# Optimization experiments

Hardware: AMD Instinct MI355X
Metric: run time of the kernel (lower is better)

## Reference

```python
import jax, jax.numpy as jnp
import numpy as np

B, S, DIN, D = 16, 1024, 64, 64

def setup_inputs() -> dict:
    key = jax.random.key(0)
    kx, kq, kk, kv, kaK, kaV = jax.random.split(key, 6)
    w_scale = 1.0 / np.sqrt(DIN)
    x = jax.random.normal(kx, (B, S, DIN), dtype=jnp.float32)
    Wq = jax.random.normal(kq, (DIN, D), dtype=jnp.float32) * w_scale
    Wk = jax.random.normal(kk, (DIN, D), dtype=jnp.float32) * w_scale
    Wv = jax.random.normal(kv, (DIN, D), dtype=jnp.float32) * w_scale
    # relative-position bias tables alpha_K/alpha_V: [S, S, D]
    alpha_K = jax.random.normal(kaK, (S, S, D), dtype=jnp.float32) * 0.02
    alpha_V = jax.random.normal(kaV, (S, S, D), dtype=jnp.float32) * 0.02
    return {"x": x, "Wq": Wq, "Wk": Wk, "Wv": Wv,
            "alpha_K": alpha_K, "alpha_V": alpha_V}

def reference(x, Wq, Wk, Wv, alpha_K, alpha_V):
    # Relation-aware self-attention (Shaw et al. style), vectorized form of
    # the original per-query loop:
    #   score[b,i,j] = q[b,i] . (k[b,j] + alpha_K[i,j]) / sqrt(D)
    #   z[b,i]       = sum_j softmax_j(score)[b,i,j] * (v[b,j] + alpha_V[i,j])
    d = Wq.shape[1]
    inv_sqrt_d = 1.0 / np.sqrt(d)
    q = jnp.einsum('bsf,fd->bsd', x, Wq)
    k = jnp.einsum('bsf,fd->bsd', x, Wk)
    v = jnp.einsum('bsf,fd->bsd', x, Wv)
    scores = (jnp.einsum('bid,bjd->bij', q, k)
              + jnp.einsum('bid,ijd->bij', q, alpha_K)) * inv_sqrt_d
    attn = jax.nn.softmax(scores, axis=-1)  # [B, S, S]
    z = (jnp.einsum('bij,bjd->bid', attn, v)
         + jnp.einsum('bij,ijd->bid', attn, alpha_V))
    return z, attn
```

## Files before the change

kernel.cpp:

```cpp
#include <hip/hip_runtime.h>
#include <hip/hip_fp16.h>
#include <hip/hip_bf16.h>


typedef unsigned short u16;
typedef __attribute__((ext_vector_type(8))) short bhalf8;
typedef __attribute__((ext_vector_type(4))) float fx4;

__device__ __forceinline__ short b16(float f) {
  __hip_bfloat16 h = __float2bfloat16(f);
  return *reinterpret_cast<short*>(&h);
}

__device__ __forceinline__ bhalf8 pack8(float4 a, float4 b) {
  bhalf8 r;
  r[0] = b16(a.x); r[1] = b16(a.y); r[2] = b16(a.z); r[3] = b16(a.w);
  r[4] = b16(b.x); r[5] = b16(b.y); r[6] = b16(b.z); r[7] = b16(b.w);
  return r;
}

__global__ __launch_bounds__(256) void k_proj(
    const float* __restrict__ x, const float* __restrict__ Wq,
    const float* __restrict__ Wk, const float* __restrict__ Wv,
    u16* __restrict__ qbf, u16* __restrict__ kbf, float* __restrict__ vf)
{
  __shared__ float wl[3 * 4096];
  const int t = threadIdx.x;
  for (int c = t; c < 4096; c += 256) {
    wl[c] = Wq[c]; wl[4096 + c] = Wk[c]; wl[8192 + c] = Wv[c];
  }
  __syncthreads();
  const int row = blockIdx.x * 64 + (t >> 2);
  const int dbase = (t & 3) * 16;
  float xr[64];
  const float4* xp = (const float4*)(x + (size_t)row * 64);
#pragma unroll
  for (int c = 0; c < 16; ++c) {
    float4 v = xp[c];
    xr[4*c] = v.x; xr[4*c+1] = v.y; xr[4*c+2] = v.z; xr[4*c+3] = v.w;
  }
  float aq[16], ak[16], av[16];
#pragma unroll
  for (int m = 0; m < 16; ++m) { aq[m] = 0.f; ak[m] = 0.f; av[m] = 0.f; }
#pragma unroll
  for (int f = 0; f < 64; ++f) {
    const float xv = xr[f];
    const float* wq = wl + f * 64 + dbase;
#pragma unroll
    for (int m = 0; m < 16; ++m) {
      aq[m] = fmaf(xv, wq[m], aq[m]);
      ak[m] = fmaf(xv, wq[4096 + m], ak[m]);
      av[m] = fmaf(xv, wq[8192 + m], av[m]);
    }
  }
  union { u16 u[16]; uint4 q[2]; } pq, pk;
#pragma unroll
  for (int m = 0; m < 16; ++m) { pq.u[m] = (u16)b16(aq[m]); pk.u[m] = (u16)b16(ak[m]); }
  const size_t o = (size_t)row * 64 + dbase;
  *(uint4*)(qbf + o) = pq.q[0]; *(uint4*)(qbf + o + 8) = pq.q[1];
  *(uint4*)(kbf + o) = pk.q[0]; *(uint4*)(kbf + o + 8) = pk.q[1];
  float4* vo = (float4*)(vf + o);
  vo[0] = make_float4(av[0], av[1], av[2], av[3]);
  vo[1] = make_float4(av[4], av[5], av[6], av[7]);
  vo[2] = make_float4(av[8], av[9], av[10], av[11]);
  vo[3] = make_float4(av[12], av[13], av[14], av[15]);
}

__global__ __launch_bounds__(256) void k_qk(
    const u16* __restrict__ qbf, const u16* __restrict__ kbf, __half* __restrict__ qkw)
{
  const int t = threadIdx.x, l = t & 63, w = t >> 6;
  const int b = blockIdx.x & 15, it = blockIdx.x >> 4;
  const int lr = l & 15, lg = l >> 4;
  const int i0 = it * 64 + w * 16;
  const u16* qp = qbf + (size_t)(b * 1024 + i0 + lr) * 64 + lg * 8;
  bhalf8 a0 = *(const bhalf8*)(qp);
  bhalf8 a1 = *(const bhalf8*)(qp + 32);
  for (int jt = 0; jt < 64; ++jt) {
    const int j0 = jt * 16;
    const u16* kp = kbf + (size_t)(b * 1024 + j0 + lr) * 64 + lg * 8;
    bhalf8 b0 = *(const bhalf8*)(kp);
    bhalf8 b1 = *(const bhalf8*)(kp + 32);
    fx4 acc = {0.f, 0.f, 0.f, 0.f};
    acc = __builtin_amdgcn_mfma_f32_16x16x32_bf16(a0, b0, acc, 0, 0, 0);
    acc = __builtin_amdgcn_mfma_f32_16x16x32_bf16(a1, b1, acc, 0, 0, 0);
#pragma unroll
    for (int r = 0; r < 4; ++r) {
      const int i = i0 + lg * 4 + r;
      qkw[((size_t)i * 16 + b) * 1024 + j0 + lr] = __float2half(acc[r]);
    }
  }
}

#define SLD2 516
#define PADJ 40
__global__ __launch_bounds__(256, 4) void k_core(
    const float* __restrict__ aK, const float* __restrict__ aV,
    const u16* __restrict__ qbf, const __half* __restrict__ qkw,
    float* __restrict__ attn_out, float* __restrict__ za)
{
  __shared__ __align__(16) float sl[16 * SLD2];
  __shared__ __align__(16) u16 vt[64 * PADJ];
  __shared__ float stats[64];
  const int i = blockIdx.x;
  const int t = threadIdx.x, l = t & 63, w = t >> 6;
  const int lr = l & 15, lg = l >> 4;

  const u16* qp = qbf + (size_t)(lr * 1024 + i) * 64 + lg * 8;
  bhalf8 a0 = *(const bhalf8*)(qp);
  bhalf8 a1 = *(const bhalf8*)(qp + 32);

  fx4 zacc = {0.f, 0.f, 0.f, 0.f};

  const int jA = t >> 4;
  const int dA = (t & 15) * 4;

  for (int h = 0; h < 2; ++h) {
    const __half* qk = qkw + (size_t)i * 16384 + h * 512;
    for (int c = t; c < 1024; c += 256) {
      const int b = c >> 6;
      const int j8 = (c & 63) * 8;
      uint4 u = *(const uint4*)(qk + (size_t)b * 1024 + j8);
      const __half2* hh = (const __half2*)&u;
      float2 f0 = __half22float2(hh[0]);
      float2 f1 = __half22float2(hh[1]);
      float2 f2 = __half22float2(hh[2]);
      float2 f3 = __half22float2(hh[3]);
      float* dst = sl + b * SLD2 + j8;
      *(float4*)(dst)     = make_float4(f0.x, f0.y, f1.x, f1.y);
      *(float4*)(dst + 4) = make_float4(f2.x, f2.y, f3.x, f3.y);
    }
    __syncthreads();

    for (int tt = 0; tt < 8; ++tt) {
      const int j0 = (w + tt * 4) * 16;
      const float* ap = aK + ((size_t)i * 1024 + h * 512 + j0 + lr) * 64 + lg * 8;
      float4 c0 = *(const float4*)(ap);
      float4 c1 = *(const float4*)(ap + 4);
      float4 c2 = *(const float4*)(ap + 32);
      float4 c3 = *(const float4*)(ap + 36);
      fx4 acc = {0.f, 0.f, 0.f, 0.f};
      acc = __builtin_amdgcn_mfma_f32_16x16x32_bf16(a0, pack8(c0, c1), acc, 0, 0, 0);
      acc = __builtin_amdgcn_mfma_f32_16x16x32_bf16(a1, pack8(c2, c3), acc, 0, 0, 0);
#pragma unroll
      for (int r = 0; r < 4; ++r)
        sl[(lg * 4 + r) * SLD2 + j0 + lr] += acc[r];
    }
    __syncthreads();

    if (h == 0) {
#pragma unroll
      for (int rr = 0; rr < 4; ++rr) {
        const int row = w * 4 + rr;
        float* rp = sl + row * SLD2;
        float4 x0 = *(const float4*)(rp + l * 8);
        float4 x1 = *(const float4*)(rp + l * 8 + 4);
        float v8[8] = {x0.x, x0.y, x0.z, x0.w, x1.x, x1.y, x1.z, x1.w};
        float mx = -3.0e30f;
#pragma unroll
        for (int c = 0; c < 8; ++c) mx = fmaxf(mx, v8[c]);
#pragma unroll
        for (int off = 32; off; off >>= 1) mx = fmaxf(mx, __shfl_xor(mx, off));
        float e8[8]; float sum = 0.f;
#pragma unroll
        for (int c = 0; c < 8; ++c) { e8[c] = __expf((v8[c] - mx) * 0.125f); sum += e8[c]; }
        float* ao = attn_out + ((size_t)row * 1024 + i) * 1024;
        *(float4*)(ao + l * 8)     = make_float4(e8[0], e8[1], e8[2], e8[3]);
        *(float4*)(ao + l * 8 + 4) = make_float4(e8[4], e8[5], e8[6], e8[7]);
        bhalf8 eb;
#pragma unroll
        for (int c = 0; c < 8; ++c) eb[c] = b16(e8[c]);
        *(bhalf8*)((u16*)rp + l * 8) = eb;
#pragma unroll
        for (int off = 32; off; off >>= 1) sum += __shfl_xor(sum, off);
        if (l == 0) { stats[row] = mx; stats[16 + row] = sum; }
      }
    } else {
#pragma unroll
      for (int rr = 0; rr < 4; ++rr) {
        const int row = w * 4 + rr;
        float* rp = sl + row * SLD2;
        float4 x0 = *(const float4*)(rp + l * 8);
        float4 x1 = *(const float4*)(rp + l * 8 + 4);
        float v8[8] = {x0.x, x0.y, x0.z, x0.w, x1.x, x1.y, x1.z, x1.w};
        float mx = -3.0e30f;
#pragma unroll
        for (int c = 0; c < 8; ++c) mx = fmaxf(mx, v8[c]);
#pragma unroll
        for (int off = 32; off; off >>= 1) mx = fmaxf(mx, __shfl_xor(mx, off));
        const float m1 = stats[row];
        const float m  = fmaxf(m1, mx);
        const float corr = __expf((m1 - m) * 0.125f);
        float e8[8]; float sum = 0.f;
#pragma unroll
        for (int c = 0; c < 8; ++c) { e8[c] = __expf((v8[c] - m) * 0.125f); sum += e8[c]; }
        bhalf8 eb;
#pragma unroll
        for (int c = 0; c < 8; ++c) eb[c] = b16(e8[c]);
        *(bhalf8*)((u16*)rp + l * 8) = eb;
#pragma unroll
        for (int off = 32; off; off >>= 1) sum += __shfl_xor(sum, off);
        const float inv = 1.0f / (stats[16 + row] * corr + sum);
        float* ao = attn_out + ((size_t)row * 1024 + i) * 1024 + 512;
        *(float4*)(ao + l * 8)     = make_float4(e8[0]*inv, e8[1]*inv, e8[2]*inv, e8[3]*inv);
        *(float4*)(ao + l * 8 + 4) = make_float4(e8[4]*inv, e8[5]*inv, e8[6]*inv, e8[7]*inv);
        if (l == 0) { stats[32 + row] = corr; stats[48 + row] = inv; }
      }
    }
    __syncthreads();

    if (h == 1) {
#pragma unroll
      for (int r = 0; r < 4; ++r) zacc[r] *= stats[32 + lg * 4 + r];
    }
    float4 pa, pb;
    {
      const float* ap = aV + ((size_t)i * 1024 + h * 512 + jA) * 64 + dA;
      pa = *(const float4*)(ap);
      pb = *(const float4*)(ap + 1024);
    }
    for (int it = 0; it < 16; ++it) {
      __syncthreads();
      vt[(dA + 0) * PADJ + jA] = (u16)b16(pa.x);
      vt[(dA + 1) * PADJ + jA] = (u16)b16(pa.y);
      vt[(dA + 2) * PADJ + jA] = (u16)b16(pa.z);
      vt[(dA + 3) * PADJ + jA] = (u16)b16(pa.w);
      vt[(dA + 0) * PADJ + jA + 16] = (u16)b16(pb.x);
      vt[(dA + 1) * PADJ + jA + 16] = (u16)b16(pb.y);
      vt[(dA + 2) * PADJ + jA + 16] = (u16)b16(pb.z);
      vt[(dA + 3) * PADJ + jA + 16] = (u16)b16(pb.w);
      if (it < 15) {
        const float* ap = aV + ((size_t)i * 1024 + h * 512 + (it + 1) * 32 + jA) * 64 + dA;
        pa = *(const float4*)(ap);
        pb = *(const float4*)(ap + 1024);
      }
      __syncthreads();
      bhalf8 ea = *(const bhalf8*)((const u16*)(sl + (size_t)lr * SLD2) + it * 32 + lg * 8);
      bhalf8 bv = *(const bhalf8*)(vt + (w * 16 + lr) * PADJ + lg * 8);
      zacc = __builtin_amdgcn_mfma_f32_16x16x32_bf16(ea, bv, zacc, 0, 0, 0);
    }
    __syncthreads();
  }

#pragma unroll
  for (int r = 0; r < 4; ++r) {
    const int b = lg * 4 + r;
    za[((size_t)i * 16 + b) * 64 + w * 16 + lr] = zacc[r] * stats[48 + b];
  }

#pragma unroll
  for (int rr = 0; rr < 4; ++rr) {
    const int row = w * 4 + rr;
    const float f = stats[32 + row] * stats[48 + row];
    float* ao = attn_out + ((size_t)row * 1024 + i) * 1024;
    float4 u0 = *(const float4*)(ao + l * 8);
    float4 u1 = *(const float4*)(ao + l * 8 + 4);
    *(float4*)(ao + l * 8)     = make_float4(u0.x*f, u0.y*f, u0.z*f, u0.w*f);
    *(float4*)(ao + l * 8 + 4) = make_float4(u1.x*f, u1.y*f, u1.z*f, u1.w*f);
  }
}

__global__ __launch_bounds__(256) void k_zv(
    const float* __restrict__ attn, const float* __restrict__ vf,
    const float* __restrict__ za, float* __restrict__ zout)
{
  __shared__ __align__(16) u16 vt[64 * 40];
  const int t = threadIdx.x, l = t & 63, w = t >> 6;
  const int b = blockIdx.x & 15, it = blockIdx.x >> 4;
  const int lr = l & 15, lg = l >> 4;
  const int iw = it * 64 + w * 16;
  fx4 acc[4];
#pragma unroll
  for (int n = 0; n < 4; ++n) acc[n] = (fx4){0.f, 0.f, 0.f, 0.f};
  const int jl = t >> 3;
  const int c0 = (t & 7) * 8;
  for (int ks = 0; ks < 32; ++ks) {
    const int j0 = ks * 32;
    const float* vp = vf + (size_t)(b * 1024 + j0 + jl) * 64 + c0;
    float4 v0 = *(const float4*)(vp);
    float4 v1 = *(const float4*)(vp + 4);
    __syncthreads();
    vt[(c0 + 0) * 40 + jl] = (u16)b16(v0.x);
    vt[(c0 + 1) * 40 + jl] = (u16)b16(v0.y);
    vt[(c0 + 2) * 40 + jl] = (u16)b16(v0.z);
    vt[(c0 + 3) * 40 + jl] = (u16)b16(v0.w);
    vt[(c0 + 4) * 40 + jl] = (u16)b16(v1.x);
    vt[(c0 + 5) * 40 + jl] = (u16)b16(v1.y);
    vt[(c0 + 6) * 40 + jl] = (u16)b16(v1.z);
    vt[(c0 + 7) * 40 + jl] = (u16)b16(v1.w);
    __syncthreads();
    const float* apr = attn + (size_t)(b * 1024 + iw + lr) * 1024 + j0 + lg * 8;
    float4 t0 = *(const float4*)(apr);
    float4 t1 = *(const float4*)(apr + 4);
    bhalf8 af = pack8(t0, t1);
#pragma unroll
    for (int n = 0; n < 4; ++n) {
      bhalf8 bf = *(const bhalf8*)(vt + (n * 16 + lr) * 40 + lg * 8);
      acc[n] = __builtin_amdgcn_mfma_f32_16x16x32_bf16(af, bf, acc[n], 0, 0, 0);
    }
  }
#pragma unroll
  for (int n = 0; n < 4; ++n) {
#pragma unroll
    for (int r = 0; r < 4; ++r) {
      const int i = iw + lg * 4 + r;
      const int dd = n * 16 + lr;
      zout[((size_t)b * 1024 + i) * 64 + dd] = acc[n][r] + za[((size_t)i * 16 + b) * 64 + dd];
    }
  }
}

extern "C" void kernel_launch(void* const* d_in, const int* in_sizes, int n_in,
                              void* d_out, int out_size, void* d_ws, size_t ws_size,
                              hipStream_t stream)
{
  const float* x  = (const float*)d_in[0];
  const float* Wq = (const float*)d_in[1];
  const float* Wk = (const float*)d_in[2];
  const float* Wv = (const float*)d_in[3];
  const float* aK = (const float*)d_in[4];
  const float* aV = (const float*)d_in[5];
  float* zout = (float*)d_out;
  float* attn_out = zout + (size_t)16 * 1024 * 64;

  char* ws = (char*)d_ws;
  u16*    qbf = (u16*)(ws);
  u16*    kbf = (u16*)(ws + (size_t)2  * 1024 * 1024);
  float*  vf  = (float*)(ws + (size_t)4  * 1024 * 1024);
  float*  za  = (float*)(ws + (size_t)8  * 1024 * 1024);
  __half* qkw = (__half*)(ws + (size_t)12 * 1024 * 1024);

  hipLaunchKernelGGL(k_proj, dim3(256),  dim3(256), 0, stream, x, Wq, Wk, Wv, qbf, kbf, vf);
  hipLaunchKernelGGL(k_qk,   dim3(256),  dim3(256), 0, stream, qbf, kbf, qkw);
  hipLaunchKernelGGL(k_core, dim3(1024), dim3(256), 0, stream, aK, aV, qbf, qkw, attn_out, za);
  hipLaunchKernelGGL(k_zv,   dim3(256),  dim3(256), 0, stream, attn_out, vf, za, zout);
}
```

Before: 225.8 us.

## Fuse QK bias load into softmax and make aV staging per-warp without barriers

The separate pass that loaded the q·k scores into shared memory, along with its barrier, is removed. The MFMA result now overwrites the tile, and the fp16 q·k values are added in registers during the softmax pass. The aV transpose staging is repartitioned so each warp writes only the 16 d-columns it later reads, which removes the two __syncthreads per iteration of the 16-step loop. This relies on intra-wavefront ordering of LDS writes and reads, and the per-warp loads are narrower (64-byte strips per row), which may reduce memory coalescing.

```diff
diff --git a/kernel.cpp b/kernel.cpp
--- a/kernel.cpp
+++ b/kernel.cpp
@@ -112,26 +112,7 @@
 
   fx4 zacc = {0.f, 0.f, 0.f, 0.f};
 
-  const int jA = t >> 4;
-  const int dA = (t & 15) * 4;
-
   for (int h = 0; h < 2; ++h) {
-    const __half* qk = qkw + (size_t)i * 16384 + h * 512;
-    for (int c = t; c < 1024; c += 256) {
-      const int b = c >> 6;
-      const int j8 = (c & 63) * 8;
-      uint4 u = *(const uint4*)(qk + (size_t)b * 1024 + j8);
-      const __half2* hh = (const __half2*)&u;
-      float2 f0 = __half22float2(hh[0]);
-      float2 f1 = __half22float2(hh[1]);
-      float2 f2 = __half22float2(hh[2]);
-      float2 f3 = __half22float2(hh[3]);
-      float* dst = sl + b * SLD2 + j8;
-      *(float4*)(dst)     = make_float4(f0.x, f0.y, f1.x, f1.y);
-      *(float4*)(dst + 4) = make_float4(f2.x, f2.y, f3.x, f3.y);
-    }
-    __syncthreads();
-
     for (int tt = 0; tt < 8; ++tt) {
       const int j0 = (w + tt * 4) * 16;
       const float* ap = aK + ((size_t)i * 1024 + h * 512 + j0 + lr) * 64 + lg * 8;
@@ -144,7 +125,7 @@
       acc = __builtin_amdgcn_mfma_f32_16x16x32_bf16(a1, pack8(c2, c3), acc, 0, 0, 0);
 #pragma unroll
       for (int r = 0; r < 4; ++r)
-        sl[(lg * 4 + r) * SLD2 + j0 + lr] += acc[r];
+        sl[(lg * 4 + r) * SLD2 + j0 + lr] = acc[r];
     }
     __syncthreads();
 
@@ -153,9 +134,16 @@
       for (int rr = 0; rr < 4; ++rr) {
         const int row = w * 4 + rr;
         float* rp = sl + row * SLD2;
+        uint4 qv = *(const uint4*)(qkw + ((size_t)i * 16 + row) * 1024 + l * 8);
+        const __half2* hh = (const __half2*)&qv;
+        float2 f0 = __half22float2(hh[0]);
+        float2 f1 = __half22float2(hh[1]);
+        float2 f2 = __half22float2(hh[2]);
+        float2 f3 = __half22float2(hh[3]);
         float4 x0 = *(const float4*)(rp + l * 8);
         float4 x1 = *(const float4*)(rp + l * 8 + 4);
-        float v8[8] = {x0.x, x0.y, x0.z, x0.w, x1.x, x1.y, x1.z, x1.w};
+        float v8[8] = {x0.x + f0.x, x0.y + f0.y, x0.z + f1.x, x0.w + f1.y,
+                       x1.x + f2.x, x1.y + f2.y, x1.z + f3.x, x1.w + f3.y};
         float mx = -3.0e30f;
 #pragma unroll
         for (int c = 0; c < 8; ++c) mx = fmaxf(mx, v8[c]);
@@ -180,9 +168,16 @@
       for (int rr = 0; rr < 4; ++rr) {
         const int row = w * 4 + rr;
         float* rp = sl + row * SLD2;
+        uint4 qv = *(const uint4*)(qkw + ((size_t)i * 16 + row) * 1024 + 512 + l * 8);
+        const __half2* hh = (const __half2*)&qv;
+        float2 f0 = __half22float2(hh[0]);
+        float2 f1 = __half22float2(hh[1]);
+        float2 f2 = __half22float2(hh[2]);
+        float2 f3 = __half22float2(hh[3]);
         float4 x0 = *(const float4*)(rp + l * 8);
         float4 x1 = *(const float4*)(rp + l * 8 + 4);
-        float v8[8] = {x0.x, x0.y, x0.z, x0.w, x1.x, x1.y, x1.z, x1.w};
+        float v8[8] = {x0.x + f0.x, x0.y + f0.y, x0.z + f1.x, x0.w + f1.y,
+                       x1.x + f2.x, x1.y + f2.y, x1.z + f3.x, x1.w + f3.y};
         float mx = -3.0e30f;
 #pragma unroll
         for (int c = 0; c < 8; ++c) mx = fmaxf(mx, v8[c]);
@@ -213,30 +208,29 @@
 #pragma unroll
       for (int r = 0; r < 4; ++r) zacc[r] *= stats[32 + lg * 4 + r];
     }
-    float4 pa, pb;
-    {
-      const float* ap = aV + ((size_t)i * 1024 + h * 512 + jA) * 64 + dA;
-      pa = *(const float4*)(ap);
-      pb = *(const float4*)(ap + 1024);
-    }
+    const int jj = l >> 2;
+    const int cc = (l & 3) * 4;
+    const float* avbase = aV + ((size_t)i * 1024 + h * 512) * 64 + w * 16 + cc;
+    float4 pa = *(const float4*)(avbase + (size_t)jj * 64);
+    float4 pb = *(const float4*)(avbase + (size_t)(jj + 16) * 64);
     for (int it = 0; it < 16; ++it) {
-      __syncthreads();
-      vt[(dA + 0) * PADJ + jA] = (u16)b16(pa.x);
-      vt[(dA + 1) * PADJ + jA] = (u16)b16(pa.y);
-      vt[(dA + 2) * PADJ + jA] = (u16)b16(pa.z);
-      vt[(dA + 3) * PADJ + jA] = (u16)b16(pa.w);
-      vt[(dA + 0) * PADJ + jA + 16] = (u16)b16(pb.x);
-      vt[(dA + 1) * PADJ + jA + 16] = (u16)b16(pb.y);
-      vt[(dA + 2) * PADJ + jA + 16] = (u16)b16(pb.z);
-      vt[(dA + 3) * PADJ + jA + 16] = (u16)b16(pb.w);
+      float4 ca = pa, cb = pb;
       if (it < 15) {
-        const float* ap = aV + ((size_t)i * 1024 + h * 512 + (it + 1) * 32 + jA) * 64 + dA;
-        pa = *(const float4*)(ap);
-        pb = *(const float4*)(ap + 1024);
+        const float* nb = avbase + (size_t)((it + 1) * 32) * 64;
+        pa = *(const float4*)(nb + (size_t)jj * 64);
+        pb = *(const float4*)(nb + (size_t)(jj + 16) * 64);
       }
-      __syncthreads();
+      u16* v0 = vt + (size_t)(w * 16 + cc) * PADJ + jj;
+      v0[0 * PADJ]      = (u16)b16(ca.x);
+      v0[1 * PADJ]      = (u16)b16(ca.y);
+      v0[2 * PADJ]      = (u16)b16(ca.z);
+      v0[3 * PADJ]      = (u16)b16(ca.w);
+      v0[0 * PADJ + 16] = (u16)b16(cb.x);
+      v0[1 * PADJ + 16] = (u16)b16(cb.y);
+      v0[2 * PADJ + 16] = (u16)b16(cb.z);
+      v0[3 * PADJ + 16] = (u16)b16(cb.w);
       bhalf8 ea = *(const bhalf8*)((const u16*)(sl + (size_t)lr * SLD2) + it * 32 + lg * 8);
-      bhalf8 bv = *(const bhalf8*)(vt + (w * 16 + lr) * PADJ + lg * 8);
+      bhalf8 bv = *(const bhalf8*)(vt + (size_t)(w * 16 + lr) * PADJ + lg * 8);
       zacc = __builtin_amdgcn_mfma_f32_16x16x32_bf16(ea, bv, zacc, 0, 0, 0);
     }
     __syncthreads();
```

Measured after the change: 226.0 us. No clear change (+0.1%).
